# Performance work log

Hardware: AMD Instinct MI355X
Metric: run time of the kernel (lower is better)

Reference implementation:

```python
import jax, jax.numpy as jnp
import numpy as np

B, A, K, M = 8, 100000, 80, 32
ALPHA, GAMMA = 0.25, 2.0


def _make_boxes(rng, n, img=800.0):
    cx = rng.uniform(0, img, n).astype(np.float32)
    cy = rng.uniform(0, img, n).astype(np.float32)
    w = rng.uniform(16, 256, n).astype(np.float32)
    h = rng.uniform(16, 256, n).astype(np.float32)
    return np.stack([cx - w / 2, cy - h / 2, cx + w / 2, cy + h / 2], axis=1)


def setup_inputs() -> dict:
    key = jax.random.key(0)
    k1, k2 = jax.random.split(key)
    rng = np.random.default_rng(0)
    classifications = jax.random.uniform(k1, (B, A, K), dtype=jnp.float32)  # forward clamps to (1e-4, 1-1e-4)
    regressions = jax.random.normal(k2, (B, A, 4), dtype=jnp.float32)
    anchors = jnp.asarray(_make_boxes(rng, A))[None]  # [1, A, 4]
    boxes = _make_boxes(rng, B * M).reshape(B, M, 4)
    labels = rng.integers(0, K, (B, M)).astype(np.float32)
    labels[:, M * 3 // 4:] = -1.0  # padded (invalid) annotations
    annotations = jnp.asarray(np.concatenate([boxes, labels[..., None]], axis=-1))  # [B, M, 5]
    return {"classifications": classifications, "regressions": regressions,
            "anchors": anchors, "annotations": annotations}


def _calc_iou(a, b):
    # a: [A,4] anchors, b: [M,4] gt boxes (xyxy)
    area = (b[:, 2] - b[:, 0]) * (b[:, 3] - b[:, 1])  # [M]
    iw = jnp.clip(jnp.minimum(a[:, 2:3], b[None, :, 2]) - jnp.maximum(a[:, 0:1], b[None, :, 0]), 0)
    ih = jnp.clip(jnp.minimum(a[:, 3:4], b[None, :, 3]) - jnp.maximum(a[:, 1:2], b[None, :, 1]), 0)
    inter = iw * ih  # [A,M]
    ua = ((a[:, 2] - a[:, 0]) * (a[:, 3] - a[:, 1]))[:, None] + area[None] - inter
    return inter / jnp.clip(ua, 1e-8)


def _per_image(classification, regression, anchor, ann):
    label = ann[:, 4]
    valid = label != -1.0
    has_ann = jnp.any(valid)

    iou = _calc_iou(anchor, ann[:, :4])           # [A,M]
    iou = jnp.where(valid[None, :], iou, -1.0)    # mask padded annotations
    iou_max = jnp.max(iou, axis=1)                # [A]
    iou_argmax = jnp.argmax(iou, axis=1)
    assigned = ann[iou_argmax]                    # [A,5]

    positive = iou_max >= 0.5
    num_pos = jnp.sum(positive.astype(jnp.float32))
    one_hot = jax.nn.one_hot(assigned[:, 4].astype(jnp.int32), K, dtype=jnp.float32)  # [A,K]

    targets = jnp.where((iou_max >= 0.4)[:, None], 0.25, -1.0)
    targets = jnp.where(positive[:, None], one_hot, targets)  # 0 for pos anchors, 1 at assigned class

    # focal loss (detectron form)
    logit = jnp.clip(classification, 1e-4, 1.0 - 1e-4)
    p = jax.nn.sigmoid(logit)
    term1 = (1.0 - p) ** GAMMA * jnp.log(p)
    term2 = -(p ** GAMMA) * jnp.where(logit >= 0.0,
                                      logit + jax.nn.softplus(-logit),
                                      jax.nn.softplus(logit))
    cls_loss = -jnp.where(targets != 0.0, ALPHA * term1, (1.0 - ALPHA) * term2)
    cls_total = jnp.sum(cls_loss) / jnp.maximum(num_pos, 0.01)

    aw = anchor[:, 2] - anchor[:, 0]
    ah = anchor[:, 3] - anchor[:, 1]
    acx = anchor[:, 0] + 0.5 * aw
    acy = anchor[:, 1] + 0.5 * ah
    gw = assigned[:, 2] - assigned[:, 0]
    gh = assigned[:, 3] - assigned[:, 1]
    gcx = assigned[:, 0] + 0.5 * gw
    gcy = assigned[:, 1] + 0.5 * gh
    gw = jnp.clip(gw, 1.0)
    gh = jnp.clip(gh, 1.0)
    t = jnp.stack([(gcx - acx) / aw, (gcy - acy) / ah,
                   jnp.log(gw / aw), jnp.log(gh / ah)], axis=1)
    t = t / jnp.array([0.1, 0.1, 0.2, 0.2], dtype=jnp.float32)
    diff = jnp.abs(t - regression)
    sl1 = jnp.where(diff <= 1.0 / 9.0, 0.5 * 9.0 * diff * diff, diff - 0.5 / 9.0)
    reg_sum = jnp.sum(jnp.where(positive[:, None], sl1, 0.0))
    reg_loss = jnp.where(num_pos > 0, reg_sum / jnp.maximum(num_pos * 4.0, 1.0), 0.0)

    cls_total = jnp.where(has_ann, cls_total, 0.0)
    reg_loss = jnp.where(has_ann, reg_loss, 0.0)
    return cls_total, reg_loss


def reference(classifications, regressions, anchors, annotations):
    cls_l, reg_l = jax.vmap(_per_image, in_axes=(0, 0, None, 0))(
        classifications, regressions, anchors[0], annotations)
    return (jnp.mean(cls_l, keepdims=True), jnp.mean(reg_l, keepdims=True))
```

## Files before the change

kernel.cpp:

```cpp
#include <hip/hip_runtime.h>

#define BB 8
#define AA 100000
#define KK 80
#define MM 32

__device__ __forceinline__ float cls_term(float c, int code, int k) {
    float x   = fminf(fmaxf(c, 1e-4f), 1.0f - 1e-4f);
    float em  = __expf(-x);
    float u   = 1.0f + em;
    float s   = __logf(u);
    float p   = __builtin_amdgcn_rcpf(u);
    float omp = 1.0f - p;
    bool use2 = (code >= 0) && (k != code);
    return use2 ? (0.75f * p * p * (x + s)) : (0.25f * omp * omp * s);
}

__global__ __launch_bounds__(256)
void focal_main(const float* __restrict__ cls,
                const float* __restrict__ reg,
                const float* __restrict__ anc,
                const float* __restrict__ ann,
                double* __restrict__ cls_sum,
                float*  __restrict__ reg_sum,
                int*    __restrict__ num_pos)
{
    const int blk = blockIdx.x;
    const int b   = blockIdx.y;
    const int t   = threadIdx.x;
    const int a0  = blk * 256;
    const int nA  = min(256, AA - a0);

    __shared__ float s_ann[MM * 5];
    __shared__ int   s_code[256];
    __shared__ float s_wred[4];
    __shared__ int   s_wnp[4];
    __shared__ float s_wrg[4];

    if (t < MM * 5) s_ann[t] = ann[b * MM * 5 + t];
    __syncthreads();

    int   code     = -1;
    float reg_part = 0.0f;
    int   pos      = 0;
    const int ai   = a0 + t;
    if (t < nA) {
        const float4 av = ((const float4*)anc)[ai];
        const float ax1 = av.x, ay1 = av.y, ax2 = av.z, ay2 = av.w;
        float best = -2.0f;
        int   bidx = 0;
        const float a_area = (ax2 - ax1) * (ay2 - ay1);
        #pragma unroll
        for (int m = 0; m < MM; ++m) {
            float bx1 = s_ann[m * 5 + 0], by1 = s_ann[m * 5 + 1];
            float bx2 = s_ann[m * 5 + 2], by2 = s_ann[m * 5 + 3];
            float lab = s_ann[m * 5 + 4];
            float area  = (bx2 - bx1) * (by2 - by1);
            float iw    = fmaxf(fminf(ax2, bx2) - fmaxf(ax1, bx1), 0.0f);
            float ih    = fmaxf(fminf(ay2, by2) - fmaxf(ay1, by1), 0.0f);
            float inter = iw * ih;
            float ua    = fmaxf(a_area + area - inter, 1e-8f);
            float iou   = inter / ua;
            if (lab == -1.0f) iou = -1.0f;
            if (iou > best) { best = iou; bidx = m; }
        }
        if (best >= 0.5f) {
            pos  = 1;
            code = (int)s_ann[bidx * 5 + 4];
            float gx1 = s_ann[bidx * 5 + 0], gy1 = s_ann[bidx * 5 + 1];
            float gx2 = s_ann[bidx * 5 + 2], gy2 = s_ann[bidx * 5 + 3];
            float aw  = ax2 - ax1,  ah  = ay2 - ay1;
            float acx = ax1 + 0.5f * aw, acy = ay1 + 0.5f * ah;
            float gw  = gx2 - gx1,  gh  = gy2 - gy1;
            float gcx = gx1 + 0.5f * gw, gcy = gy1 + 0.5f * gh;
            gw = fmaxf(gw, 1.0f); gh = fmaxf(gh, 1.0f);
            float tt0 = ((gcx - acx) / aw) / 0.1f;
            float tt1 = ((gcy - acy) / ah) / 0.1f;
            float tt2 = logf(gw / aw) / 0.2f;
            float tt3 = logf(gh / ah) / 0.2f;
            const float4 rv = ((const float4*)reg)[(size_t)b * AA + ai];
            float d0 = fabsf(tt0 - rv.x);
            float d1 = fabsf(tt1 - rv.y);
            float d2 = fabsf(tt2 - rv.z);
            float d3 = fabsf(tt3 - rv.w);
            const float th = 1.0f / 9.0f, hb = 0.5f / 9.0f;
            reg_part  = (d0 <= th ? 4.5f * d0 * d0 : d0 - hb)
                      + (d1 <= th ? 4.5f * d1 * d1 : d1 - hb)
                      + (d2 <= th ? 4.5f * d2 * d2 : d2 - hb)
                      + (d3 <= th ? 4.5f * d3 * d3 : d3 - hb);
        }
    }
    s_code[t] = code;

    {
        unsigned long long bal = __ballot(pos != 0);
        int wnp = __popcll(bal);
        float wrg = reg_part;
        #pragma unroll
        for (int off = 32; off > 0; off >>= 1) wrg += __shfl_down(wrg, off, 64);
        int wid  = t >> 6;
        int lane = t & 63;
        if (lane == 0) { s_wnp[wid] = wnp; s_wrg[wid] = wrg; }
    }
    __syncthreads();
    if (t == 0) {
        int   np = s_wnp[0] + s_wnp[1] + s_wnp[2] + s_wnp[3];
        float rg = s_wrg[0] + s_wrg[1] + s_wrg[2] + s_wrg[3];
        if (np != 0)  atomicAdd(&num_pos[b], np);
        if (rg != 0.f) atomicAdd(&reg_sum[b], rg);
    }

    const float4* c4 = (const float4*)(cls + ((size_t)b * AA + (size_t)a0) * KK);
    float part = 0.0f;
    auto body = [&](int idx4) {
        float4 v = c4[idx4];
        unsigned e  = (unsigned)idx4 * 4u;
        unsigned al = e / 80u;
        unsigned k0 = e - al * 80u;
        int ca = s_code[al];
        part += cls_term(v.x, ca, (int)k0);
        part += cls_term(v.y, ca, (int)k0 + 1);
        part += cls_term(v.z, ca, (int)k0 + 2);
        part += cls_term(v.w, ca, (int)k0 + 3);
    };
    if (nA == 256) {
        #pragma unroll 4
        for (int j = 0; j < 20; ++j) body(j * 256 + t);
    } else {
        const int limit4 = nA * (KK / 4);
        #pragma unroll 4
        for (int j = 0; j < 20; ++j) {
            int idx4 = j * 256 + t;
            if (idx4 < limit4) body(idx4);
        }
    }
    #pragma unroll
    for (int off = 32; off > 0; off >>= 1) part += __shfl_down(part, off, 64);
    if ((t & 63) == 0) s_wred[t >> 6] = part;
    __syncthreads();
    if (t == 0) {
        float tot = s_wred[0] + s_wred[1] + s_wred[2] + s_wred[3];
        atomicAdd(&cls_sum[b], (double)tot);
    }
}

__global__ void focal_final(const float* __restrict__ ann,
                            const double* __restrict__ cls_sum,
                            const float* __restrict__ reg_sum,
                            const int* __restrict__ num_pos,
                            float* __restrict__ out)
{
    __shared__ float s_c[BB], s_r[BB];
    int t = threadIdx.x;
    if (t < BB) {
        bool has = false;
        for (int m = 0; m < MM; ++m)
            has |= (ann[t * MM * 5 + m * 5 + 4] != -1.0f);
        float np   = (float)num_pos[t];
        float ctot = (float)cls_sum[t] / fmaxf(np, 0.01f);
        float rtot = (np > 0.0f) ? (reg_sum[t] / fmaxf(np * 4.0f, 1.0f)) : 0.0f;
        s_c[t] = has ? ctot : 0.0f;
        s_r[t] = has ? rtot : 0.0f;
    }
    __syncthreads();
    if (t == 0) {
        float c = 0.0f, r = 0.0f;
        for (int b = 0; b < BB; ++b) { c += s_c[b]; r += s_r[b]; }
        out[0] = c / (float)BB;
        out[1] = r / (float)BB;
    }
}

extern "C" void kernel_launch(void* const* d_in, const int* in_sizes, int n_in,
                              void* d_out, int out_size, void* d_ws, size_t ws_size,
                              hipStream_t stream) {
    const float* cls = (const float*)d_in[0];
    const float* reg = (const float*)d_in[1];
    const float* anc = (const float*)d_in[2];
    const float* ann = (const float*)d_in[3];
    float* out = (float*)d_out;

    double* cls_sum = (double*)d_ws;
    float*  reg_sum = (float*)((char*)d_ws + BB * sizeof(double));
    int*    num_pos = (int*)((char*)d_ws + BB * sizeof(double) + BB * sizeof(float));
    size_t  acc_bytes = BB * sizeof(double) + BB * sizeof(float) + BB * sizeof(int);

    (void)hipMemsetAsync(d_ws, 0, acc_bytes, stream);

    dim3 grid((AA + 255) / 256, BB);
    focal_main<<<grid, 256, 0, stream>>>(cls, reg, anc, ann,
                                         cls_sum, reg_sum, num_pos);
    focal_final<<<1, 64, 0, stream>>>(ann, cls_sum, reg_sum, num_pos, out);
}
```

Before: 399.0 us.

## Prefetch classification tiles before IoU matching and add negative-only fast path

Issues the first half of the per-block classification loads into registers before the IoU/regression phase, and the second half before processing, so global memory latency overlaps the anchor-matching compute. Adds a wave-uniform branch that uses a simpler negative-only loss term when no anchor in the wave is positive. This raises register pressure (20 float4 held live), which may reduce occupancy.

```diff
diff --git a/kernel.cpp b/kernel.cpp
--- a/kernel.cpp
+++ b/kernel.cpp
@@ -14,6 +14,16 @@
     float omp = 1.0f - p;
     bool use2 = (code >= 0) && (k != code);
     return use2 ? (0.75f * p * p * (x + s)) : (0.25f * omp * omp * s);
+}
+
+__device__ __forceinline__ float neg_term(float c) {
+    float x   = fminf(fmaxf(c, 1e-4f), 1.0f - 1e-4f);
+    float em  = __expf(-x);
+    float u   = 1.0f + em;
+    float s   = __logf(u);
+    float p   = __builtin_amdgcn_rcpf(u);
+    float omp = 1.0f - p;
+    return 0.25f * omp * omp * s;
 }
 
 __global__ __launch_bounds__(256)
@@ -30,6 +40,7 @@
     const int t   = threadIdx.x;
     const int a0  = blk * 256;
     const int nA  = min(256, AA - a0);
+    const bool full = (nA == 256);
 
     __shared__ float s_ann[MM * 5];
     __shared__ int   s_code[256];
@@ -37,15 +48,26 @@
     __shared__ int   s_wnp[4];
     __shared__ float s_wrg[4];
 
-    if (t < MM * 5) s_ann[t] = ann[b * MM * 5 + t];
-    __syncthreads();
+    float annv = 0.0f;
+    if (t < MM * 5) annv = ann[b * MM * 5 + t];
+    const int ai = a0 + t;
+    float4 av = make_float4(0.f, 0.f, 0.f, 0.f);
+    if (t < nA) av = ((const float4*)anc)[ai];
+
+    if (t < MM * 5) s_ann[t] = annv;
+    __syncthreads();
+
+    const float4* c4 = (const float4*)(cls + ((size_t)b * AA + (size_t)a0) * KK);
+    float4 v[10];
+    if (full) {
+        #pragma unroll
+        for (int j = 0; j < 10; ++j) v[j] = c4[j * 256 + t];
+    }
 
     int   code     = -1;
     float reg_part = 0.0f;
     int   pos      = 0;
-    const int ai   = a0 + t;
     if (t < nA) {
-        const float4 av = ((const float4*)anc)[ai];
         const float ax1 = av.x, ay1 = av.y, ax2 = av.z, ay2 = av.w;
         float best = -2.0f;
         int   bidx = 0;
@@ -110,30 +132,42 @@
         if (rg != 0.f) atomicAdd(&reg_sum[b], rg);
     }
 
-    const float4* c4 = (const float4*)(cls + ((size_t)b * AA + (size_t)a0) * KK);
     float part = 0.0f;
-    auto body = [&](int idx4) {
-        float4 v = c4[idx4];
+    auto process = [&](const float4 vv, int idx4) {
         unsigned e  = (unsigned)idx4 * 4u;
         unsigned al = e / 80u;
         unsigned k0 = e - al * 80u;
         int ca = s_code[al];
-        part += cls_term(v.x, ca, (int)k0);
-        part += cls_term(v.y, ca, (int)k0 + 1);
-        part += cls_term(v.z, ca, (int)k0 + 2);
-        part += cls_term(v.w, ca, (int)k0 + 3);
+        if (__ballot(ca >= 0) == 0ULL) {
+            part += neg_term(vv.x);
+            part += neg_term(vv.y);
+            part += neg_term(vv.z);
+            part += neg_term(vv.w);
+        } else {
+            part += cls_term(vv.x, ca, (int)k0);
+            part += cls_term(vv.y, ca, (int)k0 + 1);
+            part += cls_term(vv.z, ca, (int)k0 + 2);
+            part += cls_term(vv.w, ca, (int)k0 + 3);
+        }
     };
-    if (nA == 256) {
-        #pragma unroll 4
-        for (int j = 0; j < 20; ++j) body(j * 256 + t);
+
+    if (full) {
+        float4 w[10];
+        #pragma unroll
+        for (int j = 0; j < 10; ++j) w[j] = c4[(j + 10) * 256 + t];
+        #pragma unroll
+        for (int j = 0; j < 10; ++j) process(v[j], j * 256 + t);
+        #pragma unroll
+        for (int j = 0; j < 10; ++j) process(w[j], (j + 10) * 256 + t);
     } else {
         const int limit4 = nA * (KK / 4);
         #pragma unroll 4
         for (int j = 0; j < 20; ++j) {
             int idx4 = j * 256 + t;
-            if (idx4 < limit4) body(idx4);
-        }
-    }
+            if (idx4 < limit4) { float4 vv = c4[idx4]; process(vv, idx4); }
+        }
+    }
+
     #pragma unroll
     for (int off = 32; off > 0; off >>= 1) part += __shfl_down(part, off, 64);
     if ((t & 63) == 0) s_wred[t >> 6] = part;
```

New measurement: 380.1 us. 1.05x faster.
